# Kernel tuning notes

Measured on AMD Instinct MI355X. Metric: run time of the kernel, lower is better.

## Reference

```python
import jax, jax.numpy as jnp
import numpy as np

B, S, D = 2, 2048, 1024
H, DK, DV, DO = 16, 64, 64, 1024


def setup_inputs() -> dict:
    key = jax.random.key(0)
    ks = jax.random.split(key, 8)
    scale = 0.02
    return {
        "q": jax.random.normal(ks[0], (B, S, D), jnp.float32),
        "k": jax.random.normal(ks[1], (B, S, D), jnp.float32),
        "v": jax.random.normal(ks[2], (B, S, D), jnp.float32),
        "mask": jnp.zeros((B, S, S), jnp.float32),  # additive mask
        # weights stored [in, out] (torch Linear weight transposed)
        "Wq": jax.random.normal(ks[3], (D, H * DK), jnp.float32) * scale,
        "Wk": jax.random.normal(ks[4], (D, H * DK), jnp.float32) * scale,
        "Wv": jax.random.normal(ks[5], (D, H * DV), jnp.float32) * scale,
        "Wo": jax.random.normal(ks[6], (H * DV, DO), jnp.float32) * scale,
        "bo": jax.random.normal(ks[7], (DO,), jnp.float32) * scale,
    }


def reference(q, k, v, mask, Wq, Wk, Wv, Wo, bo):
    b, nq, _ = q.shape
    nk = k.shape[1]
    # projections -> [b, n, H, d]
    qh = (q @ Wq).reshape(b, nq, H, DK)
    kh = (k @ Wk).reshape(b, nk, H, DK)
    vh = (v @ Wv).reshape(b, nk, H, DV)
    # scores [H, b, nq, nk] (head-major to match torch view(-1, n, d) ordering)
    scores = jnp.einsum("bqhd,bkhd->hbqk", qh, kh) / jnp.sqrt(jnp.float32(DK))
    scores = scores + mask[None, :, :, :]  # mask.repeat(H,1,1)
    attn = jax.nn.softmax(scores, axis=-1)
    # output [b, nq, H, DV] -> [b, nq, H*DV]
    out = jnp.einsum("hbqk,bkhd->bqhd", attn, vh).reshape(b, nq, H * DV)
    out = out @ Wo + bo
    attention = attn.reshape(H * b, nq, nk)
    return attention, out
```

## Files before the change

### kernel.cpp

```cpp
#include <hip/hip_runtime.h>
#include <hip/hip_bf16.h>

typedef __hip_bfloat16 bf16;
typedef __attribute__((ext_vector_type(8))) short bh8;
typedef __attribute__((ext_vector_type(4))) float f4;

#define MFMA_BF16(a, b, c) __builtin_amdgcn_mfma_f32_16x16x32_bf16((a), (b), (c), 0, 0, 0)

union BH8U { bh8 v; bf16 e[8]; };

static const long ATTN_ELEMS = 134217728LL;

__global__ void k_detect(const unsigned short* __restrict__ q, int* __restrict__ flag) {
  __shared__ int cnt;
  if (threadIdx.x == 0) cnt = 0;
  __syncthreads();
  int c = 0;
  for (int i = threadIdx.x; i < 2048; i += 256) {
    const unsigned short u = q[2 * i];
    const int e = (u >> 7) & 0xFF;
    if (e >= 0xC0) ++c;
  }
  atomicAdd(&cnt, c);
  __syncthreads();
  if (threadIdx.x == 0) *flag = (cnt > 64) ? 1 : 0;
}

__global__ __launch_bounds__(256) void k_convert(const void* __restrict__ in,
                                                 bf16* __restrict__ out, long n,
                                                 const int* __restrict__ flagp) {
  const long idx = ((long)blockIdx.x * blockDim.x + threadIdx.x) * 8;
  if (idx >= n) return;
  if (*flagp) {
    const float* F = (const float*)in + idx;
    const float4 a = *(const float4*)F;
    const float4 b = *(const float4*)(F + 4);
    BH8U u;
    u.e[0] = __float2bfloat16(a.x); u.e[1] = __float2bfloat16(a.y);
    u.e[2] = __float2bfloat16(a.z); u.e[3] = __float2bfloat16(a.w);
    u.e[4] = __float2bfloat16(b.x); u.e[5] = __float2bfloat16(b.y);
    u.e[6] = __float2bfloat16(b.z); u.e[7] = __float2bfloat16(b.w);
    *(bh8*)(out + idx) = u.v;
  } else {
    *(bh8*)(out + idx) = *(const bh8*)((const bf16*)in + idx);
  }
}

__global__ __launch_bounds__(256) void k_transpose(const void* __restrict__ in,
                                                   bf16* __restrict__ out,
                                                   int R, int C,
                                                   const int* __restrict__ flagp) {
  __shared__ bf16 tile[64][65];
  const int f = *flagp;
  const int c0 = blockIdx.x * 64, r0 = blockIdx.y * 64;
  for (int i = threadIdx.x; i < 4096; i += 256) {
    const int r = i >> 6, c = i & 63;
    const long idx = (long)(r0 + r) * C + c0 + c;
    tile[r][c] = f ? __float2bfloat16(((const float*)in)[idx])
                   : ((const bf16*)in)[idx];
  }
  __syncthreads();
  for (int i = threadIdx.x; i < 4096; i += 256) {
    const int c = i >> 6, r = i & 63;
    out[(long)(c0 + c) * R + r0 + r] = tile[r][c];
  }
}

__global__ __launch_bounds__(256) void k_transpose_v(const bf16* __restrict__ Vp,
                                                     bf16* __restrict__ VT) {
  __shared__ bf16 tile[64][65];
  const int s0 = blockIdx.x * 64;
  const int h = blockIdx.y, b = blockIdx.z;
  for (int i = threadIdx.x; i < 4096; i += 256) {
    const int s = i >> 6, d = i & 63;
    tile[s][d] = Vp[(long)(b * 2048 + s0 + s) * 1024 + h * 64 + d];
  }
  __syncthreads();
  for (int i = threadIdx.x; i < 4096; i += 256) {
    const int d = i >> 6, s = i & 63;
    VT[((long)((b * 16 + h) * 64 + d)) * 2048 + s0 + s] = tile[s][d];
  }
}

__global__ __launch_bounds__(256) void k_gemm_bt(
    const bf16* __restrict__ A, const bf16* __restrict__ BT,
    bf16* __restrict__ C, char* __restrict__ Cext,
    const bf16* __restrict__ bias, const int* __restrict__ flagp,
    int M, int N, int K, float scale) {
  const int LD = 40;
  __shared__ bf16 As[128 * 40];
  __shared__ bf16 Bs[128 * 40];
  const int m0 = blockIdx.y * 128, n0 = blockIdx.x * 128;
  const int t = threadIdx.x;
  const int wave = t >> 6, lane = t & 63;
  const int wm = (wave >> 1) * 64, wn = (wave & 1) * 64;
  const int lr = lane & 15, lk = lane >> 4;

  const f4 fz = {0.f, 0.f, 0.f, 0.f};
  f4 acc[4][4];
#pragma unroll
  for (int i = 0; i < 4; ++i)
#pragma unroll
    for (int j = 0; j < 4; ++j) acc[i][j] = fz;

  const int srow = t >> 1;
  const int sch = (t & 1) * 16;
  const bf16* Ag = A + (long)(m0 + srow) * K + sch;
  const bf16* Bg = BT + (long)(n0 + srow) * K + sch;
  bf16* Asw = &As[srow * LD + sch];
  bf16* Bsw = &Bs[srow * LD + sch];

  for (int kb = 0; kb < K; kb += 32) {
    const bh8 a0 = *(const bh8*)(Ag + kb);
    const bh8 a1 = *(const bh8*)(Ag + kb + 8);
    const bh8 b0 = *(const bh8*)(Bg + kb);
    const bh8 b1 = *(const bh8*)(Bg + kb + 8);
    __syncthreads();
    *(bh8*)Asw = a0;
    *(bh8*)(Asw + 8) = a1;
    *(bh8*)Bsw = b0;
    *(bh8*)(Bsw + 8) = b1;
    __syncthreads();
    bh8 af[4], bfr[4];
#pragma unroll
    for (int i = 0; i < 4; ++i)
      af[i] = *(const bh8*)&As[(wm + i * 16 + lr) * LD + lk * 8];
#pragma unroll
    for (int j = 0; j < 4; ++j)
      bfr[j] = *(const bh8*)&Bs[(wn + j * 16 + lr) * LD + lk * 8];
#pragma unroll
    for (int i = 0; i < 4; ++i)
#pragma unroll
      for (int j = 0; j < 4; ++j) acc[i][j] = MFMA_BF16(af[i], bfr[j], acc[i][j]);
  }

  const int ext = (Cext != nullptr);
  const int f = ext ? *flagp : 0;
#pragma unroll
  for (int j = 0; j < 4; ++j) {
    const int n = n0 + wn + j * 16 + lr;
    const float bv = bias ? __bfloat162float(bias[n]) : 0.f;
#pragma unroll
    for (int i = 0; i < 4; ++i) {
      const int mr = m0 + wm + i * 16 + lk * 4;
#pragma unroll
      for (int r = 0; r < 4; ++r) {
        const float val = acc[i][j][r] * scale + bv;
        const long off = (long)(mr + r) * N + n;
        if (!ext) {
          C[off] = __float2bfloat16(val);
        } else if (f) {
          ((float*)Cext + ATTN_ELEMS)[off] = val;
        } else {
          ((bf16*)Cext + ATTN_ELEMS)[off] = __float2bfloat16(val);
        }
      }
    }
  }
}

__global__ __launch_bounds__(256) void k_attn(
    const bf16* __restrict__ Qp, const bf16* __restrict__ Kp,
    const bf16* __restrict__ VT, const void* __restrict__ mask,
    char* __restrict__ outbase, bf16* __restrict__ AV,
    const int* __restrict__ flagp) {
  const int S = 2048, HD = 1024;
  __shared__ bf16 Ks[64 * 72];
  __shared__ bf16 Vs[64 * 72];
  __shared__ bf16 Ps[64 * 72];
  const int q0 = blockIdx.x * 64;
  const int h = blockIdx.y, b = blockIdx.z;
  const int t = threadIdx.x;
  const int wave = t >> 6, lane = t & 63;
  const int lr = lane & 15, lk = lane >> 4;
  const int f = *flagp;

  const bf16* qbase = Qp + (long)(b * S + q0 + wave * 16 + lr) * HD + h * 64 + lk * 8;
  const bh8 qf0 = *(const bh8*)qbase;
  const bh8 qf1 = *(const bh8*)(qbase + 32);

  const int srow = t >> 2;
  const int sch = (t & 3) * 16;
  const bf16* Kg = Kp + (long)b * S * HD + h * 64;
  const bf16* Vg = VT + ((long)((b * 16 + h) * 64 + srow)) * S + sch;
  const long moff = (long)b * S * S + (long)(q0 + srow) * S + sch;
  const float* MgF = (const float*)mask + moff;
  const bf16* MgB = (const bf16*)mask + moff;

  float mrun[4], lrun[4];
#pragma unroll
  for (int r = 0; r < 4; ++r) { mrun[r] = -1e30f; lrun[r] = 0.f; }

  for (int kt = 0; kt < S / 64; ++kt) {
    __syncthreads();
    {
      const bf16* src = Kg + (long)(kt * 64 + srow) * HD + sch;
      const bh8 x0 = *(const bh8*)src;
      const bh8 x1 = *(const bh8*)(src + 8);
      *(bh8*)&Ks[srow * 72 + sch] = x0;
      *(bh8*)&Ks[srow * 72 + sch + 8] = x1;
      if (f) {
        const float* M = MgF + kt * 64;
        const float4 m0 = ((const float4*)M)[0], m1 = ((const float4*)M)[1];
        const float4 m2 = ((const float4*)M)[2], m3 = ((const float4*)M)[3];
        BH8U u0, u1;
        u0.e[0] = __float2bfloat16(m0.x); u0.e[1] = __float2bfloat16(m0.y);
        u0.e[2] = __float2bfloat16(m0.z); u0.e[3] = __float2bfloat16(m0.w);
        u0.e[4] = __float2bfloat16(m1.x); u0.e[5] = __float2bfloat16(m1.y);
        u0.e[6] = __float2bfloat16(m1.z); u0.e[7] = __float2bfloat16(m1.w);
        u1.e[0] = __float2bfloat16(m2.x); u1.e[1] = __float2bfloat16(m2.y);
        u1.e[2] = __float2bfloat16(m2.z); u1.e[3] = __float2bfloat16(m2.w);
        u1.e[4] = __float2bfloat16(m3.x); u1.e[5] = __float2bfloat16(m3.y);
        u1.e[6] = __float2bfloat16(m3.z); u1.e[7] = __float2bfloat16(m3.w);
        *(bh8*)&Ps[srow * 72 + sch] = u0.v;
        *(bh8*)&Ps[srow * 72 + sch + 8] = u1.v;
      } else {
        *(bh8*)&Ps[srow * 72 + sch] = *(const bh8*)(MgB + kt * 64);
        *(bh8*)&Ps[srow * 72 + sch + 8] = *(const bh8*)(MgB + kt * 64 + 8);
      }
    }
    __syncthreads();
    float s[4][4];
#pragma unroll
    for (int nf = 0; nf < 4; ++nf) {
      const bh8 kf0 = *(const bh8*)&Ks[(nf * 16 + lr) * 72 + lk * 8];
      const bh8 kf1 = *(const bh8*)&Ks[(nf * 16 + lr) * 72 + 32 + lk * 8];
      f4 a = {0.f, 0.f, 0.f, 0.f};
      a = MFMA_BF16(qf0, kf0, a);
      a = MFMA_BF16(qf1, kf1, a);
#pragma unroll
      for (int r = 0; r < 4; ++r) {
        const int trow = wave * 16 + lk * 4 + r;
        s[nf][r] = a[r] + __bfloat162float(Ps[trow * 72 + nf * 16 + lr]);
      }
    }
#pragma unroll
    for (int r = 0; r < 4; ++r) {
      float tm = fmaxf(fmaxf(s[0][r], s[1][r]), fmaxf(s[2][r], s[3][r]));
#pragma unroll
      for (int d = 1; d < 16; d <<= 1) tm = fmaxf(tm, __shfl_xor(tm, d, 64));
      const float mnew = fmaxf(mrun[r], tm);
      float ps = __expf(s[0][r] - mnew) + __expf(s[1][r] - mnew) +
                 __expf(s[2][r] - mnew) + __expf(s[3][r] - mnew);
#pragma unroll
      for (int d = 1; d < 16; d <<= 1) ps += __shfl_xor(ps, d, 64);
      lrun[r] = lrun[r] * __expf(mrun[r] - mnew) + ps;
      mrun[r] = mnew;
    }
  }

  float rl[4];
#pragma unroll
  for (int r = 0; r < 4; ++r) rl[r] = 1.f / lrun[r];

  const f4 fz = {0.f, 0.f, 0.f, 0.f};
  f4 oacc[4];
#pragma unroll
  for (int nf = 0; nf < 4; ++nf) oacc[nf] = fz;

  const long aoff = (long)(h * 2 + b) * S * S + (long)(q0 + srow) * S + sch;
  float* attnF = (float*)outbase + aoff;
  bf16* attnB = (bf16*)outbase + aoff;

  for (int kt = 0; kt < S / 64; ++kt) {
    __syncthreads();
    {
      const bf16* src = Kg + (long)(kt * 64 + srow) * HD + sch;
      const bh8 x0 = *(const bh8*)src;
      const bh8 x1 = *(const bh8*)(src + 8);
      const bh8 y0 = *(const bh8*)(Vg + kt * 64);
      const bh8 y1 = *(const bh8*)(Vg + kt * 64 + 8);
      *(bh8*)&Ks[srow * 72 + sch] = x0;
      *(bh8*)&Ks[srow * 72 + sch + 8] = x1;
      *(bh8*)&Vs[srow * 72 + sch] = y0;
      *(bh8*)&Vs[srow * 72 + sch + 8] = y1;
      if (f) {
        const float* M = MgF + kt * 64;
        const float4 m0 = ((const float4*)M)[0], m1 = ((const float4*)M)[1];
        const float4 m2 = ((const float4*)M)[2], m3 = ((const float4*)M)[3];
        BH8U u0, u1;
        u0.e[0] = __float2bfloat16(m0.x); u0.e[1] = __float2bfloat16(m0.y);
        u0.e[2] = __float2bfloat16(m0.z); u0.e[3] = __float2bfloat16(m0.w);
        u0.e[4] = __float2bfloat16(m1.x); u0.e[5] = __float2bfloat16(m1.y);
        u0.e[6] = __float2bfloat16(m1.z); u0.e[7] = __float2bfloat16(m1.w);
        u1.e[0] = __float2bfloat16(m2.x); u1.e[1] = __float2bfloat16(m2.y);
        u1.e[2] = __float2bfloat16(m2.z); u1.e[3] = __float2bfloat16(m2.w);
        u1.e[4] = __float2bfloat16(m3.x); u1.e[5] = __float2bfloat16(m3.y);
        u1.e[6] = __float2bfloat16(m3.z); u1.e[7] = __float2bfloat16(m3.w);
        *(bh8*)&Ps[srow * 72 + sch] = u0.v;
        *(bh8*)&Ps[srow * 72 + sch + 8] = u1.v;
      } else {
        *(bh8*)&Ps[srow * 72 + sch] = *(const bh8*)(MgB + kt * 64);
        *(bh8*)&Ps[srow * 72 + sch + 8] = *(const bh8*)(MgB + kt * 64 + 8);
      }
    }
    __syncthreads();
#pragma unroll
    for (int nf = 0; nf < 4; ++nf) {
      const bh8 kf0 = *(const bh8*)&Ks[(nf * 16 + lr) * 72 + lk * 8];
      const bh8 kf1 = *(const bh8*)&Ks[(nf * 16 + lr) * 72 + 32 + lk * 8];
      f4 a = {0.f, 0.f, 0.f, 0.f};
      a = MFMA_BF16(qf0, kf0, a);
      a = MFMA_BF16(qf1, kf1, a);
#pragma unroll
      for (int r = 0; r < 4; ++r) {
        const int trow = wave * 16 + lk * 4 + r;
        const float sv = a[r] + __bfloat162float(Ps[trow * 72 + nf * 16 + lr]);
        const float p = __expf(sv - mrun[r]) * rl[r];
        Ps[trow * 72 + nf * 16 + lr] = __float2bfloat16(p);
      }
    }
    __syncthreads();
    {
      BH8U p0, p1;
      p0.v = *(const bh8*)&Ps[srow * 72 + sch];
      p1.v = *(const bh8*)&Ps[srow * 72 + sch + 8];
      if (f) {
        float* dst = attnF + kt * 64;
        const float4 o0 = {__bfloat162float(p0.e[0]), __bfloat162float(p0.e[1]),
                           __bfloat162float(p0.e[2]), __bfloat162float(p0.e[3])};
        const float4 o1 = {__bfloat162float(p0.e[4]), __bfloat162float(p0.e[5]),
                           __bfloat162float(p0.e[6]), __bfloat162float(p0.e[7])};
        const float4 o2 = {__bfloat162float(p1.e[0]), __bfloat162float(p1.e[1]),
                           __bfloat162float(p1.e[2]), __bfloat162float(p1.e[3])};
        const float4 o3 = {__bfloat162float(p1.e[4]), __bfloat162float(p1.e[5]),
                           __bfloat162float(p1.e[6]), __bfloat162float(p1.e[7])};
        ((float4*)dst)[0] = o0;
        ((float4*)dst)[1] = o1;
        ((float4*)dst)[2] = o2;
        ((float4*)dst)[3] = o3;
      } else {
        bf16* dst = attnB + kt * 64;
        *(bh8*)dst = p0.v;
        *(bh8*)(dst + 8) = p1.v;
      }
    }
    const bh8 pa0 = *(const bh8*)&Ps[(wave * 16 + lr) * 72 + lk * 8];
    const bh8 pa1 = *(const bh8*)&Ps[(wave * 16 + lr) * 72 + 32 + lk * 8];
#pragma unroll
    for (int nf = 0; nf < 4; ++nf) {
      const bh8 vb0 = *(const bh8*)&Vs[(nf * 16 + lr) * 72 + lk * 8];
      const bh8 vb1 = *(const bh8*)&Vs[(nf * 16 + lr) * 72 + 32 + lk * 8];
      oacc[nf] = MFMA_BF16(pa0, vb0, oacc[nf]);
      oacc[nf] = MFMA_BF16(pa1, vb1, oacc[nf]);
    }
  }

#pragma unroll
  for (int nf = 0; nf < 4; ++nf) {
#pragma unroll
    for (int r = 0; r < 4; ++r) {
      const int qrow = q0 + wave * 16 + lk * 4 + r;
      AV[(long)(b * S + qrow) * HD + h * 64 + nf * 16 + lr] =
          __float2bfloat16(oacc[nf][r]);
    }
  }
}

extern "C" void kernel_launch(void* const* d_in, const int* in_sizes, int n_in,
                              void* d_out, int out_size, void* d_ws, size_t ws_size,
                              hipStream_t stream) {
  const void* q    = d_in[0];
  const void* k    = d_in[1];
  const void* v    = d_in[2];
  const void* mask = d_in[3];
  const void* Wq   = d_in[4];
  const void* Wk   = d_in[5];
  const void* Wv   = d_in[6];
  const void* Wo   = d_in[7];
  const void* bo   = d_in[8];

  char* ws = (char*)d_ws;
  const size_t MB = 1024 * 1024;
  bf16* WqT = (bf16*)(ws + 0 * MB);
  bf16* WkT = (bf16*)(ws + 2 * MB);
  bf16* WvT = (bf16*)(ws + 4 * MB);
  bf16* WoT = (bf16*)(ws + 6 * MB);
  bf16* boC = (bf16*)(ws + 8 * MB);
  int* flag = (int*)(ws + 8 * MB + 8192);
  bf16* Qp  = (bf16*)(ws + 9 * MB);
  bf16* Kp  = (bf16*)(ws + 17 * MB);
  bf16* VTr = (bf16*)(ws + 25 * MB);
  bf16* AV  = (bf16*)(ws + 33 * MB);

  char* ob = (char*)d_out;
  bf16* qc = (bf16*)(ob + 0 * MB);
  bf16* kc = (bf16*)(ob + 8 * MB);
  bf16* vc = (bf16*)(ob + 16 * MB);
  bf16* Vp = (bf16*)(ob + 24 * MB);

  k_detect<<<1, 256, 0, stream>>>((const unsigned short*)q, flag);

  const long NQKV = 4194304;
  k_convert<<<2048, 256, 0, stream>>>(q, qc, NQKV, flag);
  k_convert<<<2048, 256, 0, stream>>>(k, kc, NQKV, flag);
  k_convert<<<2048, 256, 0, stream>>>(v, vc, NQKV, flag);
  k_convert<<<1, 256, 0, stream>>>(bo, boC, 1024, flag);

  const dim3 tgrid(16, 16);
  k_transpose<<<tgrid, 256, 0, stream>>>(Wq, WqT, 1024, 1024, flag);
  k_transpose<<<tgrid, 256, 0, stream>>>(Wk, WkT, 1024, 1024, flag);
  k_transpose<<<tgrid, 256, 0, stream>>>(Wv, WvT, 1024, 1024, flag);
  k_transpose<<<tgrid, 256, 0, stream>>>(Wo, WoT, 1024, 1024, flag);

  const dim3 ggrid(8, 32);
  k_gemm_bt<<<ggrid, 256, 0, stream>>>(qc, WqT, Qp, nullptr, nullptr, flag,
                                       4096, 1024, 1024, 0.125f);
  k_gemm_bt<<<ggrid, 256, 0, stream>>>(kc, WkT, Kp, nullptr, nullptr, flag,
                                       4096, 1024, 1024, 1.0f);
  k_gemm_bt<<<ggrid, 256, 0, stream>>>(vc, WvT, Vp, nullptr, nullptr, flag,
                                       4096, 1024, 1024, 1.0f);

  k_transpose_v<<<dim3(32, 16, 2), 256, 0, stream>>>(Vp, VTr);

  k_attn<<<dim3(32, 16, 2), 256, 0, stream>>>(Qp, Kp, VTr, mask, ob, AV, flag);

  k_gemm_bt<<<ggrid, 256, 0, stream>>>(AV, WoT, nullptr, ob, boC, flag,
                                       4096, 1024, 1024, 1.0f);
}
```

Measured before the change: 1.007 ms.

## Skip mask loads when mask is all zero; batch QKV launches; nontemporal attn stores

A new kernel scans the whole additive mask once per call and sets a flag when every entry is zero. The attention kernel then runs a templated variant that skips loading, converting and adding the mask, so each head no longer re-reads the full mask. The separate convert, transpose and QKV GEMM launches are merged into single launches that use blockIdx.z to pick the tensor. The attention-probability output is written with nontemporal stores to reduce cache pollution. In exchange, every call pays for a full extra pass over the mask.

New measurement: 1.282 ms. +27.3%, slower.

```diff
diff --git a/kernel.cpp b/kernel.cpp
--- a/kernel.cpp
+++ b/kernel.cpp
@@ -23,15 +23,33 @@
   }
   atomicAdd(&cnt, c);
   __syncthreads();
-  if (threadIdx.x == 0) *flag = (cnt > 64) ? 1 : 0;
-}
-
-__global__ __launch_bounds__(256) void k_convert(const void* __restrict__ in,
-                                                 bf16* __restrict__ out, long n,
-                                                 const int* __restrict__ flagp) {
+  if (threadIdx.x == 0) {
+    flag[0] = (cnt > 64) ? 1 : 0;
+    flag[1] = 1;
+  }
+}
+
+__global__ __launch_bounds__(256) void k_maskzero(const void* __restrict__ mask,
+                                                  int* __restrict__ flag) {
+  const int f = flag[0];
+  const long nvec = f ? 2097152L : 1048576L;
+  const unsigned int mbits = f ? 0x7fffffffu : 0x7fff7fffu;
+  const uint4* W = (const uint4*)mask;
+  unsigned int acc = 0;
+  for (long i = (long)blockIdx.x * 256 + threadIdx.x; i < nvec;
+       i += (long)gridDim.x * 256) {
+    const uint4 w = W[i];
+    acc |= (w.x | w.y | w.z | w.w);
+  }
+  if (acc & mbits) flag[1] = 0;
+}
+
+__device__ __forceinline__ void convert_body(const void* __restrict__ in,
+                                             bf16* __restrict__ out, long n,
+                                             int f) {
   const long idx = ((long)blockIdx.x * blockDim.x + threadIdx.x) * 8;
   if (idx >= n) return;
-  if (*flagp) {
+  if (f) {
     const float* F = (const float*)in + idx;
     const float4 a = *(const float4*)F;
     const float4 b = *(const float4*)(F + 4);
@@ -46,11 +64,32 @@
   }
 }
 
-__global__ __launch_bounds__(256) void k_transpose(const void* __restrict__ in,
-                                                   bf16* __restrict__ out,
-                                                   int R, int C,
-                                                   const int* __restrict__ flagp) {
+__global__ __launch_bounds__(256) void k_convert(const void* __restrict__ in,
+                                                 bf16* __restrict__ out, long n,
+                                                 const int* __restrict__ flagp) {
+  convert_body(in, out, n, *flagp);
+}
+
+__global__ __launch_bounds__(256) void k_convert3(
+    const void* __restrict__ i0, const void* __restrict__ i1,
+    const void* __restrict__ i2, bf16* __restrict__ o0, bf16* __restrict__ o1,
+    bf16* __restrict__ o2, const int* __restrict__ flagp) {
+  const int z = blockIdx.z;
+  const void* in = (z == 0) ? i0 : (z == 1) ? i1 : i2;
+  bf16* out = (z == 0) ? o0 : (z == 1) ? o1 : o2;
+  convert_body(in, out, 4194304L, *flagp);
+}
+
+__global__ __launch_bounds__(256) void k_transpose4(
+    const void* __restrict__ i0, const void* __restrict__ i1,
+    const void* __restrict__ i2, const void* __restrict__ i3,
+    bf16* __restrict__ o0, bf16* __restrict__ o1, bf16* __restrict__ o2,
+    bf16* __restrict__ o3, const int* __restrict__ flagp) {
   __shared__ bf16 tile[64][65];
+  const int z = blockIdx.z;
+  const void* in = (z == 0) ? i0 : (z == 1) ? i1 : (z == 2) ? i2 : i3;
+  bf16* out = (z == 0) ? o0 : (z == 1) ? o1 : (z == 2) ? o2 : o3;
+  const int R = 1024, C = 1024;
   const int f = *flagp;
   const int c0 = blockIdx.x * 64, r0 = blockIdx.y * 64;
   for (int i = threadIdx.x; i < 4096; i += 256) {
@@ -82,14 +121,12 @@
   }
 }
 
-__global__ __launch_bounds__(256) void k_gemm_bt(
+__device__ __forceinline__ void gemm_body(
     const bf16* __restrict__ A, const bf16* __restrict__ BT,
     bf16* __restrict__ C, char* __restrict__ Cext,
     const bf16* __restrict__ bias, const int* __restrict__ flagp,
-    int M, int N, int K, float scale) {
+    int M, int N, int K, float scale, bf16* As, bf16* Bs) {
   const int LD = 40;
-  __shared__ bf16 As[128 * 40];
-  __shared__ bf16 Bs[128 * 40];
   const int m0 = blockIdx.y * 128, n0 = blockIdx.x * 128;
   const int t = threadIdx.x;
   const int wave = t >> 6, lane = t & 63;
@@ -159,21 +196,44 @@
   }
 }
 
-__global__ __launch_bounds__(256) void k_attn(
+__global__ __launch_bounds__(256) void k_gemm_bt(
+    const bf16* __restrict__ A, const bf16* __restrict__ BT,
+    bf16* __restrict__ C, char* __restrict__ Cext,
+    const bf16* __restrict__ bias, const int* __restrict__ flagp,
+    int M, int N, int K, float scale) {
+  __shared__ bf16 As[128 * 40];
+  __shared__ bf16 Bs[128 * 40];
+  gemm_body(A, BT, C, Cext, bias, flagp, M, N, K, scale, As, Bs);
+}
+
+__global__ __launch_bounds__(256) void k_gemm3(
+    const bf16* __restrict__ A0, const bf16* __restrict__ A1,
+    const bf16* __restrict__ A2, const bf16* __restrict__ B0,
+    const bf16* __restrict__ B1, const bf16* __restrict__ B2,
+    bf16* __restrict__ C0, bf16* __restrict__ C1, bf16* __restrict__ C2,
+    float s0) {
+  __shared__ bf16 As[128 * 40];
+  __shared__ bf16 Bs[128 * 40];
+  const int z = blockIdx.z;
+  const bf16* A = (z == 0) ? A0 : (z == 1) ? A1 : A2;
+  const bf16* BT = (z == 0) ? B0 : (z == 1) ? B1 : B2;
+  bf16* C = (z == 0) ? C0 : (z == 1) ? C1 : C2;
+  gemm_body(A, BT, C, nullptr, nullptr, nullptr, 4096, 1024, 1024,
+            (z == 0) ? s0 : 1.0f, As, Bs);
+}
+
+template <int MZ>
+__device__ __forceinline__ void attn_body(
     const bf16* __restrict__ Qp, const bf16* __restrict__ Kp,
     const bf16* __restrict__ VT, const void* __restrict__ mask,
-    char* __restrict__ outbase, bf16* __restrict__ AV,
-    const int* __restrict__ flagp) {
+    char* __restrict__ outbase, bf16* __restrict__ AV, const int f,
+    bf16* Ks, bf16* Vs, bf16* Ps) {
   const int S = 2048, HD = 1024;
-  __shared__ bf16 Ks[64 * 72];
-  __shared__ bf16 Vs[64 * 72];
-  __shared__ bf16 Ps[64 * 72];
   const int q0 = blockIdx.x * 64;
   const int h = blockIdx.y, b = blockIdx.z;
   const int t = threadIdx.x;
   const int wave = t >> 6, lane = t & 63;
   const int lr = lane & 15, lk = lane >> 4;
-  const int f = *flagp;
 
   const bf16* qbase = Qp + (long)(b * S + q0 + wave * 16 + lr) * HD + h * 64 + lk * 8;
   const bh8 qf0 = *(const bh8*)qbase;
@@ -199,24 +259,26 @@
       const bh8 x1 = *(const bh8*)(src + 8);
       *(bh8*)&Ks[srow * 72 + sch] = x0;
       *(bh8*)&Ks[srow * 72 + sch + 8] = x1;
-      if (f) {
-        const float* M = MgF + kt * 64;
-        const float4 m0 = ((const float4*)M)[0], m1 = ((const float4*)M)[1];
-        const float4 m2 = ((const float4*)M)[2], m3 = ((const float4*)M)[3];
-        BH8U u0, u1;
-        u0.e[0] = __float2bfloat16(m0.x); u0.e[1] = __float2bfloat16(m0.y);
-        u0.e[2] = __float2bfloat16(m0.z); u0.e[3] = __float2bfloat16(m0.w);
-        u0.e[4] = __float2bfloat16(m1.x); u0.e[5] = __float2bfloat16(m1.y);
-        u0.e[6] = __float2bfloat16(m1.z); u0.e[7] = __float2bfloat16(m1.w);
-        u1.e[0] = __float2bfloat16(m2.x); u1.e[1] = __float2bfloat16(m2.y);
-        u1.e[2] = __float2bfloat16(m2.z); u1.e[3] = __float2bfloat16(m2.w);
-        u1.e[4] = __float2bfloat16(m3.x); u1.e[5] = __float2bfloat16(m3.y);
-        u1.e[6] = __float2bfloat16(m3.z); u1.e[7] = __float2bfloat16(m3.w);
-        *(bh8*)&Ps[srow * 72 + sch] = u0.v;
-        *(bh8*)&Ps[srow * 72 + sch + 8] = u1.v;
-      } else {
-        *(bh8*)&Ps[srow * 72 + sch] = *(const bh8*)(MgB + kt * 64);
-        *(bh8*)&Ps[srow * 72 + sch + 8] = *(const bh8*)(MgB + kt * 64 + 8);
+      if (!MZ) {
+        if (f) {
+          const float* M = MgF + kt * 64;
+          const float4 m0 = ((const float4*)M)[0], m1 = ((const float4*)M)[1];
+          const float4 m2 = ((const float4*)M)[2], m3 = ((const float4*)M)[3];
+          BH8U u0, u1;
+          u0.e[0] = __float2bfloat16(m0.x); u0.e[1] = __float2bfloat16(m0.y);
+          u0.e[2] = __float2bfloat16(m0.z); u0.e[3] = __float2bfloat16(m0.w);
+          u0.e[4] = __float2bfloat16(m1.x); u0.e[5] = __float2bfloat16(m1.y);
+          u0.e[6] = __float2bfloat16(m1.z); u0.e[7] = __float2bfloat16(m1.w);
+          u1.e[0] = __float2bfloat16(m2.x); u1.e[1] = __float2bfloat16(m2.y);
+          u1.e[2] = __float2bfloat16(m2.z); u1.e[3] = __float2bfloat16(m2.w);
+          u1.e[4] = __float2bfloat16(m3.x); u1.e[5] = __float2bfloat16(m3.y);
+          u1.e[6] = __float2bfloat16(m3.z); u1.e[7] = __float2bfloat16(m3.w);
+          *(bh8*)&Ps[srow * 72 + sch] = u0.v;
+          *(bh8*)&Ps[srow * 72 + sch + 8] = u1.v;
+        } else {
+          *(bh8*)&Ps[srow * 72 + sch] = *(const bh8*)(MgB + kt * 64);
+          *(bh8*)&Ps[srow * 72 + sch + 8] = *(const bh8*)(MgB + kt * 64 + 8);
+        }
       }
     }
     __syncthreads();
@@ -231,7 +293,9 @@
 #pragma unroll
       for (int r = 0; r < 4; ++r) {
         const int trow = wave * 16 + lk * 4 + r;
-        s[nf][r] = a[r] + __bfloat162float(Ps[trow * 72 + nf * 16 + lr]);
+        float sv = a[r];
+        if (!MZ) sv += __bfloat162float(Ps[trow * 72 + nf * 16 + lr]);
+        s[nf][r] = sv;
       }
     }
 #pragma unroll
@@ -274,24 +338,26 @@
       *(bh8*)&Ks[srow * 72 + sch + 8] = x1;
       *(bh8*)&Vs[srow * 72 + sch] = y0;
       *(bh8*)&Vs[srow * 72 + sch + 8] = y1;
-      if (f) {
-        const float* M = MgF + kt * 64;
-        const float4 m0 = ((const float4*)M)[0], m1 = ((const float4*)M)[1];
-        const float4 m2 = ((const float4*)M)[2], m3 = ((const float4*)M)[3];
-        BH8U u0, u1;
-        u0.e[0] = __float2bfloat16(m0.x); u0.e[1] = __float2bfloat16(m0.y);
-        u0.e[2] = __float2bfloat16(m0.z); u0.e[3] = __float2bfloat16(m0.w);
-        u0.e[4] = __float2bfloat16(m1.x); u0.e[5] = __float2bfloat16(m1.y);
-        u0.e[6] = __float2bfloat16(m1.z); u0.e[7] = __float2bfloat16(m1.w);
-        u1.e[0] = __float2bfloat16(m2.x); u1.e[1] = __float2bfloat16(m2.y);
-        u1.e[2] = __float2bfloat16(m2.z); u1.e[3] = __float2bfloat16(m2.w);
-        u1.e[4] = __float2bfloat16(m3.x); u1.e[5] = __float2bfloat16(m3.y);
-        u1.e[6] = __float2bfloat16(m3.z); u1.e[7] = __float2bfloat16(m3.w);
-        *(bh8*)&Ps[srow * 72 + sch] = u0.v;
-        *(bh8*)&Ps[srow * 72 + sch + 8] = u1.v;
-      } else {
-        *(bh8*)&Ps[srow * 72 + sch] = *(const bh8*)(MgB + kt * 64);
-        *(bh8*)&Ps[srow * 72 + sch + 8] = *(const bh8*)(MgB + kt * 64 + 8);
+      if (!MZ) {
+        if (f) {
+          const float* M = MgF + kt * 64;
+          const float4 m0 = ((const float4*)M)[0], m1 = ((const float4*)M)[1];
+          const float4 m2 = ((const float4*)M)[2], m3 = ((const float4*)M)[3];
+          BH8U u0, u1;
+          u0.e[0] = __float2bfloat16(m0.x); u0.e[1] = __float2bfloat16(m0.y);
+          u0.e[2] = __float2bfloat16(m0.z); u0.e[3] = __float2bfloat16(m0.w);
+          u0.e[4] = __float2bfloat16(m1.x); u0.e[5] = __float2bfloat16(m1.y);
+          u0.e[6] = __float2bfloat16(m1.z); u0.e[7] = __float2bfloat16(m1.w);
+          u1.e[0] = __float2bfloat16(m2.x); u1.e[1] = __float2bfloat16(m2.y);
+          u1.e[2] = __float2bfloat16(m2.z); u1.e[3] = __float2bfloat16(m2.w);
+          u1.e[4] = __float2bfloat16(m3.x); u1.e[5] = __float2bfloat16(m3.y);
+          u1.e[6] = __float2bfloat16(m3.z); u1.e[7] = __float2bfloat16(m3.w);
+          *(bh8*)&Ps[srow * 72 + sch] = u0.v;
+          *(bh8*)&Ps[srow * 72 + sch + 8] = u1.v;
+        } else {
+          *(bh8*)&Ps[srow * 72 + sch] = *(const bh8*)(MgB + kt * 64);
+          *(bh8*)&Ps[srow * 72 + sch + 8] = *(const bh8*)(MgB + kt * 64 + 8);
+        }
       }
     }
     __syncthreads();
@@ -305,7 +371,8 @@
 #pragma unroll
       for (int r = 0; r < 4; ++r) {
         const int trow = wave * 16 + lk * 4 + r;
-        const float sv = a[r] + __bfloat162float(Ps[trow * 72 + nf * 16 + lr]);
+        float sv = a[r];
+        if (!MZ) sv += __bfloat162float(Ps[trow * 72 + nf * 16 + lr]);
         const float p = __expf(sv - mrun[r]) * rl[r];
         Ps[trow * 72 + nf * 16 + lr] = __float2bfloat16(p);
       }
@@ -317,22 +384,22 @@
       p1.v = *(const bh8*)&Ps[srow * 72 + sch + 8];
       if (f) {
         float* dst = attnF + kt * 64;
-        const float4 o0 = {__bfloat162float(p0.e[0]), __bfloat162float(p0.e[1]),
-                           __bfloat162float(p0.e[2]), __bfloat162float(p0.e[3])};
-        const float4 o1 = {__bfloat162float(p0.e[4]), __bfloat162float(p0.e[5]),
-                           __bfloat162float(p0.e[6]), __bfloat162float(p0.e[7])};
-        const float4 o2 = {__bfloat162float(p1.e[0]), __bfloat162float(p1.e[1]),
-                           __bfloat162float(p1.e[2]), __bfloat162float(p1.e[3])};
-        const float4 o3 = {__bfloat162float(p1.e[4]), __bfloat162float(p1.e[5]),
-                           __bfloat162float(p1.e[6]), __bfloat162float(p1.e[7])};
-        ((float4*)dst)[0] = o0;
-        ((float4*)dst)[1] = o1;
-        ((float4*)dst)[2] = o2;
-        ((float4*)dst)[3] = o3;
+        const f4 o0 = {__bfloat162float(p0.e[0]), __bfloat162float(p0.e[1]),
+                       __bfloat162float(p0.e[2]), __bfloat162float(p0.e[3])};
+        const f4 o1 = {__bfloat162float(p0.e[4]), __bfloat162float(p0.e[5]),
+                       __bfloat162float(p0.e[6]), __bfloat162float(p0.e[7])};
+        const f4 o2 = {__bfloat162float(p1.e[0]), __bfloat162float(p1.e[1]),
+                       __bfloat162float(p1.e[2]), __bfloat162float(p1.e[3])};
+        const f4 o3 = {__bfloat162float(p1.e[4]), __bfloat162float(p1.e[5]),
+                       __bfloat162float(p1.e[6]), __bfloat162float(p1.e[7])};
+        __builtin_nontemporal_store(o0, (f4*)dst + 0);
+        __builtin_nontemporal_store(o1, (f4*)dst + 1);
+        __builtin_nontemporal_store(o2, (f4*)dst + 2);
+        __builtin_nontemporal_store(o3, (f4*)dst + 3);
       } else {
         bf16* dst = attnB + kt * 64;
-        *(bh8*)dst = p0.v;
-        *(bh8*)(dst + 8) = p1.v;
+        __builtin_nontemporal_store(p0.v, (bh8*)dst);
+        __builtin_nontemporal_store(p1.v, (bh8*)(dst + 8));
       }
     }
     const bh8 pa0 = *(const bh8*)&Ps[(wave * 16 + lr) * 72 + lk * 8];
@@ -355,6 +422,21 @@
           __float2bfloat16(oacc[nf][r]);
     }
   }
+}
+
+__global__ __launch_bounds__(256) void k_attn(
+    const bf16* __restrict__ Qp, const bf16* __restrict__ Kp,
+    const bf16* __restrict__ VT, const void* __restrict__ mask,
+    char* __restrict__ outbase, bf16* __restrict__ AV,
+    const int* __restrict__ flagp) {
+  __shared__ bf16 Ks[64 * 72];
+  __shared__ bf16 Vs[64 * 72];
+  __shared__ bf16 Ps[64 * 72];
+  const int f = flagp[0];
+  if (flagp[1])
+    attn_body<1>(Qp, Kp, VT, mask, outbase, AV, f, Ks, Vs, Ps);
+  else
+    attn_body<0>(Qp, Kp, VT, mask, outbase, AV, f, Ks, Vs, Ps);
 }
 
 extern "C" void kernel_launch(void* const* d_in, const int* in_sizes, int n_in,
@@ -390,31 +472,22 @@
   bf16* Vp = (bf16*)(ob + 24 * MB);
 
   k_detect<<<1, 256, 0, stream>>>((const unsigned short*)q, flag);
-
-  const long NQKV = 4194304;
-  k_convert<<<2048, 256, 0, stream>>>(q, qc, NQKV, flag);
-  k_convert<<<2048, 256, 0, stream>>>(k, kc, NQKV, flag);
-  k_convert<<<2048, 256, 0, stream>>>(v, vc, NQKV, flag);
+  k_maskzero<<<2048, 256, 0, stream>>>(mask, flag);
+
+  k_convert3<<<dim3(2048, 1, 3), 256, 0, stream>>>(q, k, v, qc, kc, vc, flag);
   k_convert<<<1, 256, 0, stream>>>(bo, boC, 1024, flag);
 
-  const dim3 tgrid(16, 16);
-  k_transpose<<<tgrid, 256, 0, stream>>>(Wq, WqT, 1024, 1024, flag);
-  k_transpose<<<tgrid, 256, 0, stream>>>(Wk, WkT, 1024, 1024, flag);
-  k_transpose<<<tgrid, 256, 0, stream>>>(Wv, WvT, 1024, 1024, flag);
-  k_transpose<<<tgrid, 256, 0, stream>>>(Wo, WoT, 1024, 1024, flag);
+  k_transpose4<<<dim3(16, 16, 4), 256, 0, stream>>>(Wq, Wk, Wv, Wo, WqT, WkT,
+                                                    WvT, WoT, flag);
+
+  k_gemm3<<<dim3(8, 32, 3), 256, 0, stream>>>(qc, kc, vc, WqT, WkT, WvT, Qp, Kp,
+                                              Vp, 0.125f);
+
+  k_transpose_v<<<dim3(32, 16, 2), 256, 0, stream>>>(Vp, VTr);
+
+  k_attn<<<dim3(32, 16, 2), 256, 0, stream>>>(Qp, Kp, VTr, mask, ob, AV, flag);
 
   const dim3 ggrid(8, 32);
-  k_gemm_bt<<<ggrid, 256, 0, stream>>>(qc, WqT, Qp, nullptr, nullptr, flag,
-                                       4096, 1024, 1024, 0.125f);
-  k_gemm_bt<<<ggrid, 256, 0, stream>>>(kc, WkT, Kp, nullptr, nullptr, flag,
-                                       4096, 1024, 1024, 1.0f);
-  k_gemm_bt<<<ggrid, 256, 0, stream>>>(vc, WvT, Vp, nullptr, nullptr, flag,
-                                       4096, 1024, 1024, 1.0f);
-
-  k_transpose_v<<<dim3(32, 16, 2), 256, 0, stream>>>(Vp, VTr);
-
-  k_attn<<<dim3(32, 16, 2), 256, 0, stream>>>(Qp, Kp, VTr, mask, ob, AV, flag);
-
   k_gemm_bt<<<ggrid, 256, 0, stream>>>(AV, WoT, nullptr, ob, boC, flag,
                                        4096, 1024, 1024, 1.0f);
 }
```
